# Performance work log

Measured on AMD Instinct MI355X. Metric: run time of the kernel, lower is better.

## Reference

```python
import jax, jax.numpy as jnp
import numpy as np

EPS = 1e-6


def _feature_map(x):
    # elu(x) + 1
    return jax.nn.elu(x) + 1.0


def _causal_dot(Qb, Kb, V):
    """Causal linear attention numerator for 3 stacked branches.
    Qb, Kb: [3, N, L, H, D]; V: [N, L, H, Dv] -> out [3, N, L, H, Dv].
    out[b,n,l,h,:] = sum_{s<=l} (Qb[b,n,l,h,:] . Kb[b,n,s,h,:]) V[n,s,h,:]
    computed with an O(L) recurrent scan over cumulative KV outer products.
    """
    Qs = jnp.moveaxis(Qb, 2, 0)  # [L, 3, N, H, D]
    Ks = jnp.moveaxis(Kb, 2, 0)  # [L, 3, N, H, D]
    Vs = jnp.moveaxis(V, 1, 0)   # [L, N, H, Dv]
    B, N, _, H, D = Qb.shape
    Dv = V.shape[-1]
    S0 = jnp.zeros((B, N, H, D, Dv), dtype=Qb.dtype)

    def step(S, inp):
        q, k, v = inp  # q,k: [3,N,H,D], v: [N,H,Dv]
        S = S + k[..., :, None] * v[None, :, :, None, :]
        o = jnp.einsum('bnhi,bnhij->bnhj', q, S)
        return S, o

    _, out = jax.lax.scan(step, S0, (Qs, Ks, Vs))  # out: [L,3,N,H,Dv]
    return jnp.moveaxis(out, 0, 2)  # [3,N,L,H,Dv]


def setup_inputs() -> dict:
    key = jax.random.key(0)
    ks = jax.random.split(key, 5)
    N, L, H, D = 4, 2048, 8, 128
    return {
        'queries': jax.random.normal(ks[0], (N, L, H, D), dtype=jnp.float32),
        'q2': jax.random.normal(ks[1], (N, L, H, D), dtype=jnp.float32),
        'keys': jax.random.normal(ks[2], (N, L, H, D), dtype=jnp.float32),
        'values': jax.random.normal(ks[3], (N, L, H, D), dtype=jnp.float32),
        'key_lengths': jnp.ones((N, L), dtype=jnp.float32),
        'omega': jax.random.normal(ks[4], (H, D, D), dtype=jnp.float32),
    }


def reference(queries, q2, keys, values, key_lengths, omega):
    N, L, H, D = queries.shape
    Q = _feature_map(queries)                       # [N,L,H,D]
    K = _feature_map(keys) * key_lengths[:, :, None, None]

    # Delta[n,l,h,i] = l/L for all n,h,i -> projection through omega reduces to
    # (l/L) * sum_i omega[h,i,j], same math as einsum('nlhi,hij->nlhj', Delta, omega).
    delta = (jnp.arange(L, dtype=queries.dtype) / L)        # [L]
    t = delta[:, None, None] * jnp.sum(omega, axis=1)[None]  # [L,H,D]
    sin_t, cos_t = jnp.sin(t), jnp.cos(t)
    s2, c2, sc = sin_t ** 2, cos_t ** 2, sin_t * cos_t       # [L,H,D] each

    # Q_term = sin(phi(q2))^2 * feature_map(queries)
    q2_proj = jnp.einsum('nlhi,hij->nlhj', q2, omega)
    Q_term = (jnp.sin(q2_proj) ** 2) * Q                     # [N,L,H,D]

    # Branch trig weights: Q gets [sin^2, cos^2, sin*cos], K gets [cos^2, sin^2, sin*cos]
    wq = jnp.stack([s2, c2, sc])[:, None]  # [3,1,L,H,D]
    wk = jnp.stack([c2, s2, sc])[:, None]
    Qb = Q_term[None] * wq                 # [3,N,L,H,D]
    Kb = K[None] * wk                      # [3,N,L,H,D]

    # Denominator terms Z_b = <Q_b[l], cumsum_{s<=l} K_b[s]>
    Kcum = jnp.cumsum(Kb, axis=2)
    Z = jnp.einsum('bnlhi,bnlhi->bnlh', Qb, Kcum)   # [3,N,L,H]

    Vb = _causal_dot(Qb, Kb, values)                # [3,N,L,H,D]

    numerator = Vb[0] + Vb[1] - 2.0 * Vb[2]
    denominator = Z[0] + Z[1] - 2.0 * Z[2] + EPS
    return numerator / denominator[:, :, :, None]
```

## Files before the change

### kernel.cpp

```cpp
#include <hip/hip_runtime.h>


typedef float f32x4 __attribute__((ext_vector_type(4)));
typedef short s16x8 __attribute__((ext_vector_type(8)));
typedef short s16x4 __attribute__((ext_vector_type(4)));
typedef unsigned short u16;

static constexpr int    Ln   = 2048;
static constexpr size_t NHLD = (size_t)32 * 2048 * 128;
static constexpr size_t KSB  = (size_t)32 * 16 * 128;

__device__ __forceinline__ float b2f(u16 s) {
  union { unsigned u; float f; } x; x.u = ((unsigned)s) << 16; return x.f;
}
__device__ __forceinline__ u16 f2b(float f) {
  union { float f; unsigned u; } x; x.f = f;
  unsigned r = x.u + 0x7fffu + ((x.u >> 16) & 1u);
  return (u16)(r >> 16);
}
__device__ __forceinline__ s16x8 pack8(f32x4 a, f32x4 b) {
  s16x8 r;
  r[0] = (short)f2b(a[0]); r[1] = (short)f2b(a[1]); r[2] = (short)f2b(a[2]); r[3] = (short)f2b(a[3]);
  r[4] = (short)f2b(b[0]); r[5] = (short)f2b(b[1]); r[6] = (short)f2b(b[2]); r[7] = (short)f2b(b[3]);
  return r;
}

__global__ __launch_bounds__(256) void k_omega(const float* __restrict__ om,
                                               u16* __restrict__ wt, float* __restrict__ osum) {
  __shared__ alignas(16) u16 T[128][136];
  int h = blockIdx.x, t = threadIdx.x;
  for (int idx = t; idx < 128 * 32; idx += 256) {
    int i = idx >> 5, cs = (idx & 31) << 2;
    f32x4 vv = *(const f32x4*)(om + ((size_t)(h * 128 + i)) * 128 + cs);
    T[i][cs + 0] = f2b(vv[0]); T[i][cs + 1] = f2b(vv[1]);
    T[i][cs + 2] = f2b(vv[2]); T[i][cs + 3] = f2b(vv[3]);
  }
  if (t < 128) {
    float acc = 0.f;
    for (int i = 0; i < 128; i++) acc += om[((size_t)(h * 128 + i)) * 128 + t];
    osum[h * 128 + t] = acc;
  }
  __syncthreads();
  {
    int j = t >> 1, lh = (t & 1) << 6;
    s16x8* dst = (s16x8*)(wt + ((size_t)(h * 128 + j)) * 128 + lh);
    for (int u = 0; u < 8; u++) {
      s16x8 pv;
#pragma unroll
      for (int e = 0; e < 8; e++) pv[e] = (short)T[lh + u * 8 + e][j];
      dst[u] = pv;
    }
  }
}

__global__ __launch_bounds__(256) void k_kvfeat(const float* __restrict__ kg, const float* __restrict__ vg,
                                                const float* __restrict__ klg, const float* __restrict__ osum,
                                                u16* __restrict__ kb3, u16* __restrict__ kbt3,
                                                u16* __restrict__ vt) {
  __shared__ alignas(16) u16 T0[128][128], T1[128][128];
  int bid = blockIdx.x, t = threadIdx.x;
  int c = bid & 15, h = (bid >> 4) & 7, n = bid >> 7;
  int l0 = c << 7, nh = (n << 3) + h;
  const float invL = 1.0f / 2048.0f;
  unsigned r2p[16][2];

#pragma unroll
  for (int it = 0; it < 16; it++) {
    int idx = (it << 8) + t;
    int rr = idx >> 5, g = idx & 31, cs = g << 2;
    int l = l0 + rr;
    size_t gb = (((size_t)(n * Ln + l) * 8 + h) << 7) + cs;
    f32x4 kv = *(const f32x4*)(kg + gb);
    f32x4 osv = *(const f32x4*)(osum + h * 128 + cs);
    float klv = klg[n * Ln + l];
    float tb = (float)l * invL;
    u16 r0[4], r1[4], r2[4];
#pragma unroll
    for (int e = 0; e < 4; e++) {
      float kf = (kv[e] > 0.f ? kv[e] + 1.f : __expf(kv[e])) * klv;
      float tt = tb * osv[e];
      float s, cc; __sincosf(tt, &s, &cc);
      r0[e] = f2b(kf * cc * cc);
      r1[e] = f2b(kf * s * s);
      r2[e] = f2b(kf * s * cc);
    }
    r2p[it][0] = (unsigned)r2[0] | ((unsigned)r2[1] << 16);
    r2p[it][1] = (unsigned)r2[2] | ((unsigned)r2[3] << 16);
    int gs = (g ^ (rr >> 3)) << 2;
    *(s16x4*)&T0[rr][gs] = (s16x4){(short)r0[0], (short)r0[1], (short)r0[2], (short)r0[3]};
    *(s16x4*)&T1[rr][gs] = (s16x4){(short)r1[0], (short)r1[1], (short)r1[2], (short)r1[3]};
    size_t nb = ((size_t)nh * Ln + l) * 128 + cs;
    *(s16x4*)(kb3 + nb)          = (s16x4){(short)r0[0], (short)r0[1], (short)r0[2], (short)r0[3]};
    *(s16x4*)(kb3 + NHLD + nb)   = (s16x4){(short)r1[0], (short)r1[1], (short)r1[2], (short)r1[3]};
    *(s16x4*)(kb3 + 2*NHLD + nb) = (s16x4){(short)r2[0], (short)r2[1], (short)r2[2], (short)r2[3]};
  }
  __syncthreads();
  {
    size_t b0 = ((size_t)(nh * 16 + c)) << 14;
    size_t b1 = ((size_t)((32 + nh) * 16 + c)) << 14;
    for (int idx = t; idx < 2048; idx += 256) {
      int i = idx >> 4, o = idx & 15;
      int gp = (((i >> 2) ^ o) << 2) + (i & 3);
      s16x8 v0, v1;
#pragma unroll
      for (int u = 0; u < 8; u++) {
        int r = (o << 3) + u;
        v0[u] = (short)T0[r][gp];
        v1[u] = (short)T1[r][gp];
      }
      size_t off = (((size_t)i) << 7) + (o << 3);
      *(s16x8*)(kbt3 + b0 + off) = v0;
      *(s16x8*)(kbt3 + b1 + off) = v1;
    }
  }
  __syncthreads();
#pragma unroll
  for (int it = 0; it < 16; it++) {
    int idx = (it << 8) + t;
    int rr = idx >> 5, g = idx & 31, cs = g << 2;
    int l = l0 + rr;
    size_t gb = (((size_t)(n * Ln + l) * 8 + h) << 7) + cs;
    f32x4 vv = *(const f32x4*)(vg + gb);
    int gs = (g ^ (rr >> 3)) << 2;
    *(s16x4*)&T1[rr][gs] = (s16x4){(short)f2b(vv[0]), (short)f2b(vv[1]),
                                   (short)f2b(vv[2]), (short)f2b(vv[3])};
    *(unsigned*)&T0[rr][gs]     = r2p[it][0];
    *(unsigned*)&T0[rr][gs + 2] = r2p[it][1];
  }
  __syncthreads();
  {
    size_t b2 = ((size_t)((64 + nh) * 16 + c)) << 14;
    size_t bv = ((size_t)(nh * 16 + c)) << 14;
    for (int idx = t; idx < 2048; idx += 256) {
      int i = idx >> 4, o = idx & 15;
      int gp = (((i >> 2) ^ o) << 2) + (i & 3);
      s16x8 v0, v1;
#pragma unroll
      for (int u = 0; u < 8; u++) {
        int r = (o << 3) + u;
        v0[u] = (short)T0[r][gp];
        v1[u] = (short)T1[r][gp];
      }
      size_t off = (((size_t)i) << 7) + (o << 3);
      *(s16x8*)(kbt3 + b2 + off) = v0;
      *(s16x8*)(vt   + bv + off) = v1;
    }
  }
}

__global__ __launch_bounds__(512, 4) void p1a(const u16* __restrict__ vtg, const u16* __restrict__ kbt3,
                                              u16* __restrict__ sct, float* __restrict__ ksum) {
  __shared__ alignas(16) u16 B[128][136];
  int bid = blockIdx.x, t = threadIdx.x;
  int c = bid & 15, h = (bid >> 4) & 7, n = (bid >> 7) & 3, b = bid >> 9;
  int nh = (n << 3) + h, bnh = b * 32 + nh;
  int lane = t & 63, quad = lane >> 4, nl = lane & 15, w = t >> 6;
  size_t tbase = ((size_t)(bnh * 16 + c)) << 14;
  for (int idx = t; idx < 2048; idx += 512) {
    *(s16x8*)&B[idx >> 4][(idx & 15) << 3] = *(const s16x8*)(kbt3 + tbase + ((size_t)idx << 3));
  }
  __syncthreads();
  f32x4 z4 = {0.f, 0.f, 0.f, 0.f};
  f32x4 acc[8];
#pragma unroll
  for (int i = 0; i < 8; i++) acc[i] = z4;
  int arow = (w << 4) + nl;
  size_t vbase = ((size_t)(nh * 16 + c)) << 14;
  for (int ks = 0; ks < 4; ks++) {
    int k0 = (ks << 5) + (quad << 3);
    s16x8 av = *(const s16x8*)(vtg + vbase + ((size_t)arow << 7) + k0);
#pragma unroll
    for (int ct = 0; ct < 8; ct++) {
      s16x8 bv = *(const s16x8*)&B[(ct << 4) + nl][k0];
      acc[ct] = __builtin_amdgcn_mfma_f32_16x16x32_bf16(av, bv, acc[ct], 0, 0, 0);
    }
  }
  if (t < 128) {
    float s = 0.f;
#pragma unroll 4
    for (int g = 0; g < 128; g += 8) {
      s16x8 v = *(const s16x8*)&B[t][g];
#pragma unroll
      for (int e = 0; e < 8; e++) s += b2f((u16)v[e]);
    }
    ksum[(size_t)(bnh * 16 + c) * 128 + t] = s;
  }
  __syncthreads();
  {
    int lbase = (w << 4) + (quad << 2);
#pragma unroll
    for (int ct = 0; ct < 8; ct++) {
      int i = (ct << 4) + nl;
#pragma unroll
      for (int r = 0; r < 4; r++) B[lbase + r][i] = f2b(acc[ct][r]);
    }
  }
  __syncthreads();
  size_t sbase = ((size_t)(bnh * 16 + c)) << 14;
  for (int idx = t; idx < 2048; idx += 512) {
    int jr = idx >> 4, g = (idx & 15) << 3;
    *(s16x8*)(sct + sbase + ((size_t)jr << 7) + g) = *(const s16x8*)&B[jr][g];
  }
}

__global__ __launch_bounds__(256) void p1b(u16* __restrict__ sct, float* __restrict__ ksum) {
  int bid = blockIdx.x, t = threadIdx.x;
  if (bid < 768) {
    int tid = bid * 256 + t;
    int bnh = tid >> 11, rem = tid & 2047;
    size_t base = ((size_t)bnh << 18) + ((size_t)rem << 3);
    float acc[8] = {0.f, 0.f, 0.f, 0.f, 0.f, 0.f, 0.f, 0.f};
    for (int c = 0; c < 16; c++) {
      size_t a = base + ((size_t)c << 14);
      s16x8 v = *(const s16x8*)(sct + a);
      s16x8 o;
#pragma unroll
      for (int e = 0; e < 8; e++) { o[e] = (short)f2b(acc[e]); acc[e] += b2f((u16)v[e]); }
      *(s16x8*)(sct + a) = o;
    }
  } else {
    int m2 = (bid - 768) * 256 + t;
    int i = m2 & 127, bnh = m2 >> 7;
    size_t base = (size_t)bnh * 2048 + i;
    float acc = 0.f;
    for (int c = 0; c < 16; c++) {
      size_t a = base + (size_t)c * 128;
      float v = ksum[a];
      ksum[a] = acc;
      acc += v;
    }
  }
}

__global__ __launch_bounds__(256, 2) void k_qfeat(const float* __restrict__ q2g, const float* __restrict__ qg,
                                                  const u16* __restrict__ wt, const float* __restrict__ osum,
                                                  const float* __restrict__ kspre,
                                                  u16* __restrict__ qb3, float* __restrict__ zintg) {
  __shared__ alignas(16) u16 B[128][136];
  __shared__ float osb[128];
  int bid = blockIdx.x, t = threadIdx.x;
  int m = bid & 31, h = (bid >> 5) & 7, n = bid >> 8;
  int l0 = m << 6, c = m >> 1, nh = (n << 3) + h;
  if (t < 128) osb[t] = osum[h * 128 + t];
  for (int idx = t; idx < 2048; idx += 256) {
    int j = idx >> 4, cs = (idx & 15) << 3;
    *(s16x8*)&B[j][cs] = *(const s16x8*)(wt + ((size_t)(h * 128 + j)) * 128 + cs);
  }
  __syncthreads();
  int lane = t & 63, quad = lane >> 4, nl = lane & 15, w = t >> 6;
  f32x4 z4 = {0.f, 0.f, 0.f, 0.f};
  f32x4 acc[8];
#pragma unroll
  for (int i = 0; i < 8; i++) acc[i] = z4;
  int arow = l0 + (w << 4) + nl;
  for (int ks = 0; ks < 4; ks++) {
    int k0 = (ks << 5) + (quad << 3);
    const float* ap = q2g + (((size_t)(n * Ln + arow) * 8 + h) << 7) + k0;
    s16x8 av = pack8(*(const f32x4*)ap, *(const f32x4*)(ap + 4));
#pragma unroll
    for (int ct = 0; ct < 8; ct++) {
      s16x8 bv = *(const s16x8*)&B[(ct << 4) + nl][k0];
      acc[ct] = __builtin_amdgcn_mfma_f32_16x16x32_bf16(av, bv, acc[ct], 0, 0, 0);
    }
  }
  __syncthreads();
  {
    int lbase = (w << 4) + (quad << 2);
#pragma unroll
    for (int ct = 0; ct < 8; ct++) {
      int j = (ct << 4) + nl;
#pragma unroll
      for (int r = 0; r < 4; r++) {
        float sp = __sinf(acc[ct][r]);
        B[lbase + r][j] = f2b(sp * sp);
      }
    }
  }
  __syncthreads();
  const float invL = 1.0f / 2048.0f;
  for (int idx = t; idx < 1024; idx += 256) {
    int l = idx >> 4, j0 = (idx & 15) << 3, gl = l0 + l;
    s16x8 s2v = *(const s16x8*)&B[l][j0];
    const float* qp = qg + (((size_t)(n * Ln + gl) * 8 + h) << 7) + j0;
    f32x4 qa = *(const f32x4*)qp, qbv = *(const f32x4*)(qp + 4);
    size_t kbb = ((size_t)nh * 16 + c) * 128 + j0;
    f32x4 kp0a = *(const f32x4*)(kspre + kbb),           kp0b = *(const f32x4*)(kspre + kbb + 4);
    f32x4 kp1a = *(const f32x4*)(kspre + kbb + KSB),     kp1b = *(const f32x4*)(kspre + kbb + KSB + 4);
    f32x4 kp2a = *(const f32x4*)(kspre + kbb + 2 * KSB), kp2b = *(const f32x4*)(kspre + kbb + 2 * KSB + 4);
    s16x8 o0, o1, o2;
    float z = 0.f;
    float tb = (float)gl * invL;
#pragma unroll
    for (int e = 0; e < 8; e++) {
      float s2p = b2f((u16)s2v[e]);
      float qv = (e < 4) ? qa[e] : qbv[e - 4];
      float f = qv > 0.f ? qv + 1.f : __expf(qv);
      float Qt = s2p * f;
      float tt = tb * osb[j0 + e];
      float s, cc; __sincosf(tt, &s, &cc);
      float v0 = Qt * s * s, v1 = Qt * cc * cc, v2 = -2.f * Qt * s * cc;
      float k0v = (e < 4) ? kp0a[e] : kp0b[e - 4];
      float k1v = (e < 4) ? kp1a[e] : kp1b[e - 4];
      float k2v = (e < 4) ? kp2a[e] : kp2b[e - 4];
      z += v0 * k0v + v1 * k1v + v2 * k2v;
      o0[e] = (short)f2b(v0); o1[e] = (short)f2b(v1); o2[e] = (short)f2b(v2);
    }
    size_t base = ((size_t)nh * Ln + gl) * 128 + j0;
    *(s16x8*)(qb3 + base)            = o0;
    *(s16x8*)(qb3 + base + NHLD)     = o1;
    *(s16x8*)(qb3 + base + 2 * NHLD) = o2;
    z += __shfl_xor(z, 1); z += __shfl_xor(z, 2);
    z += __shfl_xor(z, 4); z += __shfl_xor(z, 8);
    if (nl == 0) zintg[(size_t)nh * Ln + gl] = z;
  }
}

__global__ __launch_bounds__(512, 4) void p3(const u16* __restrict__ qb3, const u16* __restrict__ kb3,
                                             const u16* __restrict__ vtg, const u16* __restrict__ sct,
                                             const float* __restrict__ zintg, float* __restrict__ outg) {
  __shared__ union {
    struct { alignas(16) u16 T0[128][136]; alignas(16) u16 T1[128][136]; } s;
    alignas(16) float O[128][132];
  } sm;
  int bid = blockIdx.x, t = threadIdx.x;
  int c = bid & 15, h = (bid >> 4) & 7, n = bid >> 7;
  int l0c = c << 7, nh = (n << 3) + h;
  int lane = t & 63, quad = lane >> 4, nl = lane & 15, w = t >> 6;
  f32x4 z4 = {0.f, 0.f, 0.f, 0.f};
  f32x4 accP[8], accO[8];
#pragma unroll
  for (int i = 0; i < 8; i++) { accP[i] = z4; accO[i] = z4; }
  int arow = l0c + (w << 4) + nl;
  for (int b = 0; b < 3; b++) {
    int bnh = b * 32 + nh;
    __syncthreads();
    for (int idx = t; idx < 2048; idx += 512) {
      int s = idx >> 4, cs = (idx & 15) << 3;
      *(s16x8*)&sm.s.T0[s][cs] = *(const s16x8*)(kb3 + (((size_t)bnh * Ln + l0c + s) << 7) + cs);
    }
    size_t sbase = ((size_t)(bnh * 16 + c)) << 14;
    for (int idx = t; idx < 2048; idx += 512) {
      int j = idx >> 4, cs = (idx & 15) << 3;
      *(s16x8*)&sm.s.T1[j][cs] = *(const s16x8*)(sct + sbase + ((size_t)j << 7) + cs);
    }
    __syncthreads();
    s16x8 av[4];
#pragma unroll
    for (int ks = 0; ks < 4; ks++)
      av[ks] = *(const s16x8*)(qb3 + (((size_t)bnh * Ln + arow) << 7) + (ks << 5) + (quad << 3));
    for (int ks = 0; ks < 4; ks++) {
      int k0 = (ks << 5) + (quad << 3);
#pragma unroll
      for (int ct = 0; ct < 8; ct++) {
        s16x8 bv0 = *(const s16x8*)&sm.s.T0[(ct << 4) + nl][k0];
        accP[ct] = __builtin_amdgcn_mfma_f32_16x16x32_bf16(av[ks], bv0, accP[ct], 0, 0, 0);
        s16x8 bv1 = *(const s16x8*)&sm.s.T1[(ct << 4) + nl][k0];
        accO[ct] = __builtin_amdgcn_mfma_f32_16x16x32_bf16(av[ks], bv1, accO[ct], 0, 0, 0);
      }
    }
  }
  __syncthreads();
  float zP[4] = {0.f, 0.f, 0.f, 0.f};
  int lbase = (w << 4) + (quad << 2);
#pragma unroll
  for (int ct = 0; ct < 8; ct++) {
    int ss = (ct << 4) + nl;
#pragma unroll
    for (int r = 0; r < 4; r++) {
      int lr = lbase + r;
      float pv = (ss <= lr) ? accP[ct][r] : 0.f;
      zP[r] += pv;
      sm.s.T0[lr][ss] = f2b(pv);
    }
  }
#pragma unroll
  for (int mteam = 1; mteam <= 8; mteam <<= 1) {
#pragma unroll
    for (int r = 0; r < 4; r++) zP[r] += __shfl_xor(zP[r], mteam);
  }
  size_t vbase = ((size_t)(nh * 16 + c)) << 14;
  for (int idx = t; idx < 2048; idx += 512) {
    *(s16x8*)&sm.s.T1[idx >> 4][(idx & 15) << 3] = *(const s16x8*)(vtg + vbase + ((size_t)idx << 3));
  }
  float zf[4];
#pragma unroll
  for (int r = 0; r < 4; r++)
    zf[r] = zintg[(size_t)nh * Ln + l0c + lbase + r] + zP[r] + 1e-6f;
  __syncthreads();
  for (int ks = 0; ks < 4; ks++) {
    int k0 = (ks << 5) + (quad << 3);
    s16x8 pav = *(const s16x8*)&sm.s.T0[(w << 4) + nl][k0];
#pragma unroll
    for (int ct = 0; ct < 8; ct++) {
      s16x8 vv = *(const s16x8*)&sm.s.T1[(ct << 4) + nl][k0];
      accO[ct] = __builtin_amdgcn_mfma_f32_16x16x32_bf16(pav, vv, accO[ct], 0, 0, 0);
    }
  }
  __syncthreads();
#pragma unroll
  for (int ct = 0; ct < 8; ct++) {
    int j = (ct << 4) + nl;
#pragma unroll
    for (int r = 0; r < 4; r++) sm.O[lbase + r][j] = accO[ct][r] / zf[r];
  }
  __syncthreads();
  for (int idx = t; idx < 4096; idx += 512) {
    int l = idx >> 5, g = (idx & 31) << 2;
    *(f32x4*)(outg + (((size_t)(n * Ln + l0c + l) * 8 + h) << 7) + g) = *(const f32x4*)&sm.O[l][g];
  }
}

extern "C" void kernel_launch(void* const* d_in, const int* in_sizes, int n_in,
                              void* d_out, int out_size, void* d_ws, size_t ws_size,
                              hipStream_t stream) {
  (void)in_sizes; (void)n_in; (void)out_size; (void)ws_size;
  const float* q   = (const float*)d_in[0];
  const float* q2  = (const float*)d_in[1];
  const float* kk  = (const float*)d_in[2];
  const float* vv  = (const float*)d_in[3];
  const float* kl  = (const float*)d_in[4];
  const float* om  = (const float*)d_in[5];
  float* out = (float*)d_out;

  u16* W     = (u16*)d_ws;
  u16* qb3   = W;
  u16* kb3   = W + 3 * NHLD;
  u16* kbt3  = W + 6 * NHLD;
  u16* vt    = W + 9 * NHLD;
  u16* sct   = W + 10 * NHLD;
  u16* wt    = W + 13 * NHLD;
  float* ks  = (float*)(W + 13 * NHLD + 131072);
  float* osm = ks + 196608;
  float* zin = osm + 1024;

  k_omega <<<8,    256, 0, stream>>>(om, wt, osm);
  k_kvfeat<<<512,  256, 0, stream>>>(kk, vv, kl, osm, kb3, kbt3, vt);
  p1a     <<<1536, 512, 0, stream>>>(vt, kbt3, sct, ks);
  p1b     <<<816,  256, 0, stream>>>(sct, ks);
  k_qfeat <<<1024, 256, 0, stream>>>(q2, q, wt, osm, ks, qb3, zin);
  p3      <<<512,  512, 0, stream>>>(qb3, kb3, vt, sct, zin, out);
}
```

Measured before the change: 277.6 us.

## Drop transposed K buffer; transpose K in p1a shared memory instead

k_kvfeat no longer writes a separate transposed copy of the three K branches (kbt3). It keeps only the row-major kb3 plus the transposed V, using one LDS tile and a single pass. p1a now loads kb3 tiles and transposes them into LDS with an XOR swizzle, and adjusts its MFMA B-operand and ksum reads to match. This removes about three NHLD bf16 arrays of global writes and their later reads. In exchange p1a does scalar 16-bit LDS scatter writes, which may cause bank conflicts, and the V operand load is now issued inside the inner loop.

```diff
diff --git a/kernel.cpp b/kernel.cpp
--- a/kernel.cpp
+++ b/kernel.cpp
@@ -55,23 +55,22 @@
 
 __global__ __launch_bounds__(256) void k_kvfeat(const float* __restrict__ kg, const float* __restrict__ vg,
                                                 const float* __restrict__ klg, const float* __restrict__ osum,
-                                                u16* __restrict__ kb3, u16* __restrict__ kbt3,
-                                                u16* __restrict__ vt) {
-  __shared__ alignas(16) u16 T0[128][128], T1[128][128];
+                                                u16* __restrict__ kb3, u16* __restrict__ vt) {
+  __shared__ alignas(16) u16 T[128][128];
   int bid = blockIdx.x, t = threadIdx.x;
   int c = bid & 15, h = (bid >> 4) & 7, n = bid >> 7;
   int l0 = c << 7, nh = (n << 3) + h;
   const float invL = 1.0f / 2048.0f;
-  unsigned r2p[16][2];
-
+  int gcol = t & 31, cs = gcol << 2;
+  f32x4 osv = *(const f32x4*)(osum + h * 128 + cs);
 #pragma unroll
   for (int it = 0; it < 16; it++) {
     int idx = (it << 8) + t;
-    int rr = idx >> 5, g = idx & 31, cs = g << 2;
+    int rr = idx >> 5;
     int l = l0 + rr;
     size_t gb = (((size_t)(n * Ln + l) * 8 + h) << 7) + cs;
     f32x4 kv = *(const f32x4*)(kg + gb);
-    f32x4 osv = *(const f32x4*)(osum + h * 128 + cs);
+    f32x4 vv = *(const f32x4*)(vg + gb);
     float klv = klg[n * Ln + l];
     float tb = (float)l * invL;
     u16 r0[4], r1[4], r2[4];
@@ -84,11 +83,9 @@
       r1[e] = f2b(kf * s * s);
       r2[e] = f2b(kf * s * cc);
     }
-    r2p[it][0] = (unsigned)r2[0] | ((unsigned)r2[1] << 16);
-    r2p[it][1] = (unsigned)r2[2] | ((unsigned)r2[3] << 16);
-    int gs = (g ^ (rr >> 3)) << 2;
-    *(s16x4*)&T0[rr][gs] = (s16x4){(short)r0[0], (short)r0[1], (short)r0[2], (short)r0[3]};
-    *(s16x4*)&T1[rr][gs] = (s16x4){(short)r1[0], (short)r1[1], (short)r1[2], (short)r1[3]};
+    int gs = (gcol ^ (rr >> 3)) << 2;
+    *(s16x4*)&T[rr][gs] = (s16x4){(short)f2b(vv[0]), (short)f2b(vv[1]),
+                                  (short)f2b(vv[2]), (short)f2b(vv[3])};
     size_t nb = ((size_t)nh * Ln + l) * 128 + cs;
     *(s16x4*)(kb3 + nb)          = (s16x4){(short)r0[0], (short)r0[1], (short)r0[2], (short)r0[3]};
     *(s16x4*)(kb3 + NHLD + nb)   = (s16x4){(short)r1[0], (short)r1[1], (short)r1[2], (short)r1[3]};
@@ -96,68 +93,32 @@
   }
   __syncthreads();
   {
-    size_t b0 = ((size_t)(nh * 16 + c)) << 14;
-    size_t b1 = ((size_t)((32 + nh) * 16 + c)) << 14;
-    for (int idx = t; idx < 2048; idx += 256) {
-      int i = idx >> 4, o = idx & 15;
-      int gp = (((i >> 2) ^ o) << 2) + (i & 3);
-      s16x8 v0, v1;
-#pragma unroll
-      for (int u = 0; u < 8; u++) {
-        int r = (o << 3) + u;
-        v0[u] = (short)T0[r][gp];
-        v1[u] = (short)T1[r][gp];
-      }
-      size_t off = (((size_t)i) << 7) + (o << 3);
-      *(s16x8*)(kbt3 + b0 + off) = v0;
-      *(s16x8*)(kbt3 + b1 + off) = v1;
-    }
-  }
-  __syncthreads();
-#pragma unroll
-  for (int it = 0; it < 16; it++) {
-    int idx = (it << 8) + t;
-    int rr = idx >> 5, g = idx & 31, cs = g << 2;
-    int l = l0 + rr;
-    size_t gb = (((size_t)(n * Ln + l) * 8 + h) << 7) + cs;
-    f32x4 vv = *(const f32x4*)(vg + gb);
-    int gs = (g ^ (rr >> 3)) << 2;
-    *(s16x4*)&T1[rr][gs] = (s16x4){(short)f2b(vv[0]), (short)f2b(vv[1]),
-                                   (short)f2b(vv[2]), (short)f2b(vv[3])};
-    *(unsigned*)&T0[rr][gs]     = r2p[it][0];
-    *(unsigned*)&T0[rr][gs + 2] = r2p[it][1];
-  }
-  __syncthreads();
-  {
-    size_t b2 = ((size_t)((64 + nh) * 16 + c)) << 14;
     size_t bv = ((size_t)(nh * 16 + c)) << 14;
     for (int idx = t; idx < 2048; idx += 256) {
       int i = idx >> 4, o = idx & 15;
       int gp = (((i >> 2) ^ o) << 2) + (i & 3);
-      s16x8 v0, v1;
-#pragma unroll
-      for (int u = 0; u < 8; u++) {
-        int r = (o << 3) + u;
-        v0[u] = (short)T0[r][gp];
-        v1[u] = (short)T1[r][gp];
-      }
-      size_t off = (((size_t)i) << 7) + (o << 3);
-      *(s16x8*)(kbt3 + b2 + off) = v0;
-      *(s16x8*)(vt   + bv + off) = v1;
-    }
-  }
-}
-
-__global__ __launch_bounds__(512, 4) void p1a(const u16* __restrict__ vtg, const u16* __restrict__ kbt3,
+      s16x8 v1;
+#pragma unroll
+      for (int u = 0; u < 8; u++) v1[u] = (short)T[(o << 3) + u][gp];
+      *(s16x8*)(vt + bv + (((size_t)i) << 7) + (o << 3)) = v1;
+    }
+  }
+}
+
+__global__ __launch_bounds__(512, 4) void p1a(const u16* __restrict__ vtg, const u16* __restrict__ kb3,
                                               u16* __restrict__ sct, float* __restrict__ ksum) {
   __shared__ alignas(16) u16 B[128][136];
   int bid = blockIdx.x, t = threadIdx.x;
   int c = bid & 15, h = (bid >> 4) & 7, n = (bid >> 7) & 3, b = bid >> 9;
-  int nh = (n << 3) + h, bnh = b * 32 + nh;
+  int l0 = c << 7, nh = (n << 3) + h, bnh = b * 32 + nh;
   int lane = t & 63, quad = lane >> 4, nl = lane & 15, w = t >> 6;
-  size_t tbase = ((size_t)(bnh * 16 + c)) << 14;
+  const u16* kb = kb3 + (size_t)b * NHLD + ((size_t)nh * Ln + l0) * 128;
   for (int idx = t; idx < 2048; idx += 512) {
-    *(s16x8*)&B[idx >> 4][(idx & 15) << 3] = *(const s16x8*)(kbt3 + tbase + ((size_t)idx << 3));
+    int s = idx >> 4, io = idx & 15;
+    s16x8 v = *(const s16x8*)(kb + (((size_t)s) << 7) + (io << 3));
+    int cp = s ^ ((io & 7) << 3);
+#pragma unroll
+    for (int j = 0; j < 8; j++) B[(io << 3) + j][cp] = (u16)(short)v[j];
   }
   __syncthreads();
   f32x4 z4 = {0.f, 0.f, 0.f, 0.f};
@@ -168,18 +129,21 @@
   size_t vbase = ((size_t)(nh * 16 + c)) << 14;
   for (int ks = 0; ks < 4; ks++) {
     int k0 = (ks << 5) + (quad << 3);
-    s16x8 av = *(const s16x8*)(vtg + vbase + ((size_t)arow << 7) + k0);
 #pragma unroll
     for (int ct = 0; ct < 8; ct++) {
-      s16x8 bv = *(const s16x8*)&B[(ct << 4) + nl][k0];
+      int r = (ct << 4) + nl;
+      int koff = k0 ^ (((r >> 3) & 7) << 3);
+      s16x8 bv = *(const s16x8*)&B[r][koff];
+      s16x8 av = *(const s16x8*)(vtg + vbase + (((size_t)arow) << 7) + k0);
       acc[ct] = __builtin_amdgcn_mfma_f32_16x16x32_bf16(av, bv, acc[ct], 0, 0, 0);
     }
   }
   if (t < 128) {
     float s = 0.f;
+    int sw = ((t >> 3) & 7) << 3;
 #pragma unroll 4
     for (int g = 0; g < 128; g += 8) {
-      s16x8 v = *(const s16x8*)&B[t][g];
+      s16x8 v = *(const s16x8*)&B[t][g ^ sw];
 #pragma unroll
       for (int e = 0; e < 8; e++) s += b2f((u16)v[e]);
     }
@@ -425,7 +389,6 @@
   u16* W     = (u16*)d_ws;
   u16* qb3   = W;
   u16* kb3   = W + 3 * NHLD;
-  u16* kbt3  = W + 6 * NHLD;
   u16* vt    = W + 9 * NHLD;
   u16* sct   = W + 10 * NHLD;
   u16* wt    = W + 13 * NHLD;
@@ -434,8 +397,8 @@
   float* zin = osm + 1024;
 
   k_omega <<<8,    256, 0, stream>>>(om, wt, osm);
-  k_kvfeat<<<512,  256, 0, stream>>>(kk, vv, kl, osm, kb3, kbt3, vt);
-  p1a     <<<1536, 512, 0, stream>>>(vt, kbt3, sct, ks);
+  k_kvfeat<<<512,  256, 0, stream>>>(kk, vv, kl, osm, kb3, vt);
+  p1a     <<<1536, 512, 0, stream>>>(vt, kb3, sct, ks);
   p1b     <<<816,  256, 0, stream>>>(sct, ks);
   k_qfeat <<<1024, 256, 0, stream>>>(q2, q, wt, osm, ks, qb3, zin);
   p3      <<<512,  512, 0, stream>>>(qb3, kb3, vt, sct, zin, out);
```

Measured after the change: 270.9 us. 2.4% less time.
